# Optimization experiments

Hardware: AMD Instinct MI355X
Metric: run time of the kernel (lower is better)

The kernel has to match this reference:

```python
import jax, jax.numpy as jnp
import numpy as np
import math

E = 1024
H = 16
D = E // H  # head_dim = 64


def setup_inputs() -> dict:
    key = jax.random.key(0)
    ks = jax.random.split(key, 12)
    B, N = 2, 2048
    x = jax.random.normal(ks[0], (B, N, E), dtype=jnp.float32)
    region_mask = jax.random.randint(ks[1], (B, N), 0, 2).astype(jnp.float32)
    attn_mask = jax.random.randint(ks[2], (B, N, N), 0, 2).astype(bool)
    std = 0.02
    Wq = jax.random.normal(ks[3], (E, E), dtype=jnp.float32) * std
    Wk = jax.random.normal(ks[4], (E, E), dtype=jnp.float32) * std
    Wv = jax.random.normal(ks[5], (E, E), dtype=jnp.float32) * std
    Wo = jax.random.normal(ks[6], (E, E), dtype=jnp.float32) * std
    bq = jnp.zeros((E,), jnp.float32)
    bk = jnp.zeros((E,), jnp.float32)
    bv = jnp.zeros((E,), jnp.float32)
    bo = jnp.zeros((E,), jnp.float32)
    region_bias = jax.random.normal(ks[7], (1, H, 1, 1), dtype=jnp.float32) * std
    return {"x": x, "region_mask": region_mask, "attn_mask": attn_mask,
            "Wq": Wq, "bq": bq, "Wk": Wk, "bk": bk, "Wv": Wv, "bv": bv,
            "Wo": Wo, "bo": bo, "region_bias": region_bias}


def reference(x, region_mask, attn_mask, Wq, bq, Wk, bk, Wv, bv, Wo, bo, region_bias):
    B, N, _ = x.shape
    # projections (torch Linear: y = x @ W.T + b), split heads -> (B, H, N, D)
    def split_heads(y):
        return y.reshape(B, N, H, D).transpose(0, 2, 1, 3)
    q = split_heads(x @ Wq.T + bq)
    k = split_heads(x @ Wk.T + bk)
    v = split_heads(x @ Wv.T + bv)
    # eager scores (B, H, N, N)
    scores = jnp.einsum('bhqd,bhkd->bhqk', q, k) / math.sqrt(D)
    # additive regional bias: (1,H,1,1) * (B,1,N,1) broadcasts over keys
    scores = scores + region_bias * region_mask[:, None, :, None]
    # masked_fill(attn_mask, -inf); mask is (B,N,N) -> (B,1,N,N)
    scores = jnp.where(attn_mask[:, None, :, :], -jnp.inf, scores)
    w = jax.nn.softmax(scores, axis=-1)  # dropout is identity in eval
    out = jnp.einsum('bhqk,bhkd->bhqd', w, v)
    out = out.transpose(0, 2, 1, 3).reshape(B, N, E)
    return out @ Wo.T + bo
```

## Files before the change

### kernel.cpp

```cpp
#include <hip/hip_runtime.h>
#include <hip/hip_bf16.h>
#include <stdint.h>

typedef __hip_bfloat16 bf16;
typedef unsigned long long u64;
typedef __attribute__((ext_vector_type(4))) float f32x4;
typedef __attribute__((ext_vector_type(8))) short short8;

#define MFMA16 __builtin_amdgcn_mfma_f32_16x16x32_bf16

constexpr int Bc = 2, Nc = 2048, Ec = 1024, Hc = 16, Dc = 64;
constexpr int Mc = Bc * Nc;
constexpr int Kc = Ec;

constexpr size_t OFF_XB   = 256;
constexpr size_t SZ_XE    = (size_t)Mc * Ec * 2;
constexpr size_t SZ_W     = (size_t)Ec * Ec * 2;
constexpr size_t OFF_WQB  = OFF_XB  + SZ_XE;
constexpr size_t OFF_WKB  = OFF_WQB + SZ_W;
constexpr size_t OFF_WVB  = OFF_WKB + SZ_W;
constexpr size_t OFF_WOB  = OFF_WVB + SZ_W;
constexpr size_t OFF_QB   = OFF_WOB + SZ_W;
constexpr size_t OFF_KB   = OFF_QB  + SZ_XE;
constexpr size_t OFF_VTB  = OFF_KB  + SZ_XE;
constexpr size_t OFF_OB   = OFF_VTB + SZ_XE;
constexpr size_t OFF_MP   = OFF_OB  + SZ_XE;

#define QSCALE 0.18033688f

__device__ __forceinline__ void gld16(const void* g, void* l) {
  __builtin_amdgcn_global_load_lds((const __attribute__((address_space(1))) void*)g,
                                   (__attribute__((address_space(3))) void*)l,
                                   16, 0, 0);
}

__device__ __forceinline__ float fexp2(float x) {
#if __has_builtin(__builtin_amdgcn_exp2f)
  return __builtin_amdgcn_exp2f(x);
#else
  float r; asm("v_exp_f32 %0, %1" : "=v"(r) : "v"(x)); return r;
#endif
}

__device__ __forceinline__ unsigned cvt2(float a, float b) {
  __hip_bfloat162 h = __float22bfloat162_rn(float2{a, b});
  return *reinterpret_cast<unsigned*>(&h);
}

__device__ __forceinline__ unsigned nib4(unsigned x) {
  const unsigned b = ((x & 0x7F7F7F7Fu) + 0x7F7F7F7Fu) | x;
  return ((b >> 7) & 1u) | ((b >> 14) & 2u) | ((b >> 21) & 4u) | ((b >> 28) & 8u);
}

__global__ __launch_bounds__(256)
void prep(const unsigned char* __restrict__ mbytes,
          const float* __restrict__ x,  const float* __restrict__ wq,
          const float* __restrict__ wk, const float* __restrict__ wv,
          const float* __restrict__ wo,
          u64* __restrict__ packed,
          uint2* __restrict__ xb,  uint2* __restrict__ wqb,
          uint2* __restrict__ wkb, uint2* __restrict__ wvb,
          uint2* __restrict__ wob)
{
  if (blockIdx.x < 512) {
    __shared__ int found;
    if (threadIdx.x == 0) found = 0;
    __syncthreads();
    int loc = 0;
    for (int i = threadIdx.x; i < 4096; i += 256)
      if ((i & 3) && mbytes[i] == 1) loc = 1;
    if (loc) atomicOr(&found, 1);
    __syncthreads();
    const bool bytem = (found != 0);

    const int widx = blockIdx.x * 256 + threadIdx.x;
    u64 bits = 0;
    if (bytem) {
      const uint4* src = (const uint4*)(mbytes + (size_t)widx * 64);
#pragma unroll
      for (int i = 0; i < 4; ++i) {
        const uint4 v = src[i];
        bits |= (u64)nib4(v.x) << (16 * i + 0);
        bits |= (u64)nib4(v.y) << (16 * i + 4);
        bits |= (u64)nib4(v.z) << (16 * i + 8);
        bits |= (u64)nib4(v.w) << (16 * i + 12);
      }
    } else {
      const uint4* src = (const uint4*)mbytes + (size_t)widx * 16;
#pragma unroll
      for (int i = 0; i < 16; ++i) {
        const uint4 v = src[i];
        const unsigned n = (v.x != 0 ? 1u : 0u) | (v.y != 0 ? 2u : 0u) |
                           (v.z != 0 ? 4u : 0u) | (v.w != 0 ? 8u : 0u);
        bits |= (u64)n << (4 * i);
      }
    }
    packed[widx] = bits;
    return;
  }
  const long XG = (long)Mc * Ec / 4;
  const long WG = (long)Ec * Ec / 4;
  const long total = XG + 4 * WG;
  const long nthr = (long)(gridDim.x - 512) * 256;
  for (long g = (long)(blockIdx.x - 512) * 256 + threadIdx.x; g < total; g += nthr) {
    const float* src; uint2* dst; long r;
    if (g < XG)              { src = x;  dst = xb;  r = g; }
    else if (g < XG + WG)    { src = wq; dst = wqb; r = g - XG; }
    else if (g < XG + 2*WG)  { src = wk; dst = wkb; r = g - XG - WG; }
    else if (g < XG + 3*WG)  { src = wv; dst = wvb; r = g - XG - 2*WG; }
    else                     { src = wo; dst = wob; r = g - XG - 3*WG; }
    float4 v = reinterpret_cast<const float4*>(src)[r];
    uint2 o;
    o.x = cvt2(v.x, v.y);
    o.y = cvt2(v.z, v.w);
    dst[r] = o;
  }
}

__global__ __launch_bounds__(256)
void gemm_qkv(const bf16* __restrict__ xb,
              const bf16* __restrict__ wq, const bf16* __restrict__ wk,
              const bf16* __restrict__ wv,
              const float* __restrict__ bq, const float* __restrict__ bk,
              const float* __restrict__ bv,
              bf16* __restrict__ Q, bf16* __restrict__ Ko, bf16* __restrict__ VT)
{
  __shared__ bf16 As[2][128 * 64];
  __shared__ bf16 Bs[2][3][64 * 64];
  const int bm = blockIdx.x >> 4, bn = blockIdx.x & 15;
  const int t = threadIdx.x, lane = t & 63, w = t >> 6;
  const int wr = w >> 1, wc = w & 1;
  const int llo = lane & 15, lhi = lane >> 4;
  const int srow = t >> 3, schunk = t & 7;
  const int sswz = schunk ^ (srow & 7);
  const bf16* aSrc  = xb + (size_t)(bm * 128 + srow) * Kc + sswz * 8;
  const bf16* bSrc0 = wq + (size_t)(bn * 64 + srow) * Kc + sswz * 8;
  const bf16* bSrc1 = wk + (size_t)(bn * 64 + srow) * Kc + sswz * 8;
  const bf16* bSrc2 = wv + (size_t)(bn * 64 + srow) * Kc + sswz * 8;

  f32x4 acc[3][4][2] = {};

  auto stage = [&](int buf, int kt) {
    char* ldsA = (char*)As[buf] + w * 1024;
#pragma unroll
    for (int i = 0; i < 4; ++i)
      gld16(aSrc + (size_t)i * 32 * Kc + kt, ldsA + i * 4096);
#pragma unroll
    for (int s = 0; s < 3; ++s) {
      const bf16* bs = s == 0 ? bSrc0 : (s == 1 ? bSrc1 : bSrc2);
      char* ldsB = (char*)Bs[buf][s] + w * 1024;
      gld16(bs + kt, ldsB);
      gld16(bs + (size_t)32 * Kc + kt, ldsB + 4096);
    }
  };

  stage(0, 0);
  __syncthreads();

  for (int kti = 0; kti < Kc / 64; ++kti) {
    const int cur = kti & 1;
    if (kti + 1 < Kc / 64) stage(cur ^ 1, (kti + 1) * 64);
    const char* Asc = (const char*)As[cur];
#pragma unroll
    for (int kk = 0; kk < 2; ++kk) {
      const int chunk = (kk * 4 + lhi) ^ (lane & 7);
      short8 af[4];
#pragma unroll
      for (int i = 0; i < 4; ++i) {
        const int rowa = wr * 64 + i * 16 + llo;
        af[i] = *(const short8*)(Asc + rowa * 128 + chunk * 16);
      }
#pragma unroll
      for (int s = 0; s < 3; ++s) {
        const char* Bsc = (const char*)Bs[cur][s];
        const int rowb0 = wc * 32 + llo;
        short8 bg0 = *(const short8*)(Bsc + rowb0 * 128 + chunk * 16);
        short8 bg1 = *(const short8*)(Bsc + (rowb0 + 16) * 128 + chunk * 16);
#pragma unroll
        for (int i = 0; i < 4; ++i) {
          acc[s][i][0] = MFMA16(af[i], bg0, acc[s][i][0], 0, 0, 0);
          acc[s][i][1] = MFMA16(af[i], bg1, acc[s][i][1], 0, 0, 0);
        }
      }
    }
    __syncthreads();
  }

#pragma unroll
  for (int s = 0; s < 3; ++s) {
    const float* bias = s == 0 ? bq : (s == 1 ? bk : bv);
#pragma unroll
    for (int i = 0; i < 4; ++i)
#pragma unroll
      for (int j = 0; j < 2; ++j)
#pragma unroll
        for (int r = 0; r < 4; ++r) {
          const int m = bm * 128 + wr * 64 + i * 16 + lhi * 4 + r;
          const int e = bn * 64 + wc * 32 + j * 16 + llo;
          float v = acc[s][i][j][r] + bias[e];
          if (s == 0) {
            Q[(size_t)m * Ec + e] = __float2bfloat16(v * QSCALE);
          } else if (s == 1) {
            Ko[(size_t)m * Ec + e] = __float2bfloat16(v);
          } else {
            const int b = m >> 11, n = m & 2047, h = e >> 6, d = e & 63;
            VT[(((size_t)(b * Hc + h)) * Dc + d) * Nc + n] = __float2bfloat16(v);
          }
        }
  }
}

template<int BN>
__device__ __forceinline__ void gemm_core(const bf16* __restrict__ A,
                                          const bf16* __restrict__ Bw,
                                          int bm, int bn,
                                          bf16* As0, bf16* As1,
                                          bf16* Bs0, bf16* Bs1,
                                          f32x4 (&acc)[4][BN / 32])
{
  constexpr int NJ = BN / 32;
  const int t = threadIdx.x, lane = t & 63, w = t >> 6;
  const int wr = w >> 1, wc = w & 1;
  const int llo = lane & 15, lhi = lane >> 4;
  const int srow = t >> 3, schunk = t & 7;
  const int sswz = schunk ^ (srow & 7);
  const bf16* aSrc = A  + (size_t)(bm * 128 + srow) * Kc + sswz * 8;
  const bf16* bSrc = Bw + (size_t)(bn * BN  + srow) * Kc + sswz * 8;

  auto stage = [&](bf16* Asb, bf16* Bsb, int kt) {
    char* ldsA = (char*)Asb + w * 1024;
    char* ldsB = (char*)Bsb + w * 1024;
#pragma unroll
    for (int i = 0; i < 4; ++i)
      gld16(aSrc + (size_t)i * 32 * Kc + kt, ldsA + i * 4096);
#pragma unroll
    for (int i = 0; i < BN / 32; ++i)
      gld16(bSrc + (size_t)i * 32 * Kc + kt, ldsB + i * 4096);
  };

  stage(As0, Bs0, 0);
  __syncthreads();

  for (int kti = 0; kti < Kc / 64; ++kti) {
    const bool even = !(kti & 1);
    const char* Asc = (const char*)(even ? As0 : As1);
    const char* Bsc = (const char*)(even ? Bs0 : Bs1);
    if (kti + 1 < Kc / 64)
      stage(even ? As1 : As0, even ? Bs1 : Bs0, (kti + 1) * 64);
#pragma unroll
    for (int kk = 0; kk < 2; ++kk) {
      short8 af[4], bg[NJ];
      const int chunk = (kk * 4 + lhi) ^ (lane & 7);
#pragma unroll
      for (int i = 0; i < 4; ++i) {
        const int rowa = wr * 64 + i * 16 + llo;
        af[i] = *(const short8*)(Asc + rowa * 128 + chunk * 16);
      }
#pragma unroll
      for (int j = 0; j < NJ; ++j) {
        const int rowb = wc * (BN / 2) + j * 16 + llo;
        bg[j] = *(const short8*)(Bsc + rowb * 128 + chunk * 16);
      }
#pragma unroll
      for (int i = 0; i < 4; ++i)
#pragma unroll
        for (int j = 0; j < NJ; ++j)
          acc[i][j] = MFMA16(af[i], bg[j], acc[i][j], 0, 0, 0);
    }
    __syncthreads();
  }
}

__global__ __launch_bounds__(256)
void gemm_out(const bf16* __restrict__ ob, const bf16* __restrict__ wo,
              const float* __restrict__ bo, float* __restrict__ out)
{
  __shared__ bf16 As[2][128 * 64], Bs[2][64 * 64];
  const int bm = blockIdx.x >> 4, bn = blockIdx.x & 15;
  f32x4 acc[4][2] = {};
  gemm_core<64>(ob, wo, bm, bn, As[0], As[1], Bs[0], Bs[1], acc);

  const int t = threadIdx.x, lane = t & 63, w = t >> 6;
  const int wr = w >> 1, wc = w & 1;
  const int llo = lane & 15, lhi = lane >> 4;
#pragma unroll
  for (int i = 0; i < 4; ++i)
#pragma unroll
    for (int j = 0; j < 2; ++j)
#pragma unroll
      for (int r = 0; r < 4; ++r) {
        const int m = bm * 128 + wr * 64 + i * 16 + lhi * 4 + r;
        const int e = bn * 64 + wc * 32 + j * 16 + llo;
        out[(size_t)m * Ec + e] = acc[i][j][r] + bo[e];
      }
}

__global__ __launch_bounds__(512, 4)
void flash_attn(const bf16* __restrict__ Q, const bf16* __restrict__ Kb,
                const bf16* __restrict__ VT, const u64* __restrict__ mpack,
                bf16* __restrict__ O)
{
  __shared__ bf16 Ks[2][64 * 64];
  __shared__ bf16 Vs[2][64 * 64];
  __shared__ bf16 Ps[8][16 * 64];
  const int t = threadIdx.x, lane = t & 63, w = t >> 6;
  const int bh = blockIdx.x >> 4, qt = blockIdx.x & 15;
  const int b = bh >> 4, h = bh & 15;
  const int q0 = qt * 128 + w * 16;
  const int llo = lane & 15, lhi = lane >> 4;
  const int swz = (lane & 7) << 4;

  short8 aq0, aq1;
  {
    const bf16* qb = Q + ((size_t)(b * Nc + q0 + llo)) * Ec + h * Dc + lhi * 8;
    aq0 = *(const short8*)qb;
    aq1 = *(const short8*)(qb + 32);
  }

  const short8 kOnes = {16256,16256,16256,16256,16256,16256,16256,16256};
  const f32x4 fz = {};
  f32x4 oacc[4] = {};
  f32x4 lacc = {};

  const int srow = t >> 3, schunk = t & 7;
  const int sswz = schunk ^ (srow & 7);
  const bf16* kSrc = Kb + ((size_t)(b * Nc + srow)) * Ec + h * Dc + sswz * 8;
  const bf16* vSrc = VT + ((size_t)(bh * Dc + srow)) * Nc + sswz * 8;

  const u64* mrow = mpack + ((size_t)(b * Nc) + q0 + llo) * (Nc / 64);

  auto stage = [&](int buf, int kt) {
    gld16(kSrc + (size_t)kt * Ec, (char*)Ks[buf] + w * 1024);
    gld16(vSrc + kt,              (char*)Vs[buf] + w * 1024);
  };

  char* prow = (char*)Ps[w] + llo * 128;

  auto body = [&](const char* KsC, const char* VsC, u64 mw) {
    f32x4 s[4];
    __builtin_amdgcn_s_setprio(1);
#pragma unroll
    for (int f = 0; f < 4; ++f) {
      const int row = f * 16 + llo;
      short8 kb0 = *(const short8*)(KsC + row * 128 + (((0 + lhi) * 16) ^ swz));
      short8 kb1 = *(const short8*)(KsC + row * 128 + (((4 + lhi) * 16) ^ swz));
      s[f] = MFMA16(kb0, aq0, fz, 0, 0, 0);
      s[f] = MFMA16(kb1, aq1, s[f], 0, 0, 0);
    }
    __builtin_amdgcn_s_setprio(0);

    const unsigned mlo = (unsigned)(mw >> (lhi * 4));
    const unsigned mhi = (unsigned)(mw >> (lhi * 4 + 32));
#pragma unroll
    for (int f = 0; f < 4; ++f) {
      const unsigned mf = (f < 2 ? (mlo >> (f * 16)) : (mhi >> ((f - 2) * 16)));
#pragma unroll
      for (int r = 0; r < 4; ++r) {
        const float p = fexp2(s[f][r]);
        s[f][r] = ((mf >> r) & 1u) ? 0.f : p;
      }
    }

#pragma unroll
    for (int f = 0; f < 4; ++f) {
      uint2 pk;
      pk.x = cvt2(s[f][0], s[f][1]);
      pk.y = cvt2(s[f][2], s[f][3]);
      *(uint2*)(prow + ((f * 32 + lhi * 8) ^ swz)) = pk;
    }
    asm volatile("s_waitcnt lgkmcnt(0)" ::: "memory");

    short8 pa0 = *(const short8*)(prow + ((0 * 64 + lhi * 16) ^ swz));
    short8 pa1 = *(const short8*)(prow + ((1 * 64 + lhi * 16) ^ swz));

    __builtin_amdgcn_s_setprio(1);
#pragma unroll
    for (int df = 0; df < 4; ++df) {
      const int row = df * 16 + llo;
      short8 vb0 = *(const short8*)(VsC + row * 128 + (((0 + lhi) * 16) ^ swz));
      short8 vb1 = *(const short8*)(VsC + row * 128 + (((4 + lhi) * 16) ^ swz));
      oacc[df] = MFMA16(pa0, vb0, oacc[df], 0, 0, 0);
      oacc[df] = MFMA16(pa1, vb1, oacc[df], 0, 0, 0);
    }
    lacc = MFMA16(pa0, kOnes, lacc, 0, 0, 0);
    lacc = MFMA16(pa1, kOnes, lacc, 0, 0, 0);
    __builtin_amdgcn_s_setprio(0);
  };

  stage(0, 0);
  __syncthreads();
  u64 mw = mrow[0];

  for (int ti = 0; ti < Nc / 64; ti += 2) {
    if (ti + 1 < Nc / 64) stage(1, (ti + 1) * 64);
    const u64 mwB = (ti + 1 < Nc / 64) ? mrow[ti + 1] : 0;
    body((const char*)Ks[0], (const char*)Vs[0], mw);
    __syncthreads();
    if (ti + 2 < Nc / 64) stage(0, (ti + 2) * 64);
    const u64 mwA = (ti + 2 < Nc / 64) ? mrow[ti + 2] : 0;
    body((const char*)Ks[1], (const char*)Vs[1], mwB);
    __syncthreads();
    mw = mwA;
  }

  float inv[4];
#pragma unroll
  for (int r = 0; r < 4; ++r) inv[r] = 1.0f / lacc[r];
#pragma unroll
  for (int df = 0; df < 4; ++df)
#pragma unroll
    for (int r = 0; r < 4; ++r) {
      const int q = q0 + lhi * 4 + r;
      const int e = h * Dc + df * 16 + llo;
      O[((size_t)(b * Nc + q)) * Ec + e] = __float2bfloat16(oacc[df][r] * inv[r]);
    }
}

extern "C" void kernel_launch(void* const* d_in, const int* in_sizes, int n_in,
                              void* d_out, int out_size, void* d_ws, size_t ws_size,
                              hipStream_t stream)
{
  (void)in_sizes; (void)n_in; (void)out_size; (void)ws_size;
  const float* x  = (const float*)d_in[0];
  const void* mask = d_in[2];
  const float* Wq = (const float*)d_in[3];
  const float* bq = (const float*)d_in[4];
  const float* Wk = (const float*)d_in[5];
  const float* bk = (const float*)d_in[6];
  const float* Wv = (const float*)d_in[7];
  const float* bv = (const float*)d_in[8];
  const float* Wo = (const float*)d_in[9];
  const float* bo = (const float*)d_in[10];
  float* out = (float*)d_out;
  char* ws = (char*)d_ws;

  bf16* XB  = (bf16*)(ws + OFF_XB);
  bf16* WQB = (bf16*)(ws + OFF_WQB);
  bf16* WKB = (bf16*)(ws + OFF_WKB);
  bf16* WVB = (bf16*)(ws + OFF_WVB);
  bf16* WOB = (bf16*)(ws + OFF_WOB);
  bf16* QB  = (bf16*)(ws + OFF_QB);
  bf16* KB  = (bf16*)(ws + OFF_KB);
  bf16* VTB = (bf16*)(ws + OFF_VTB);
  bf16* OB  = (bf16*)(ws + OFF_OB);
  u64*  MP  = (u64*)(ws + OFF_MP);

  prep<<<512 + 1280, 256, 0, stream>>>((const unsigned char*)mask,
                                       x, Wq, Wk, Wv, Wo, MP,
                                       (uint2*)XB, (uint2*)WQB, (uint2*)WKB,
                                       (uint2*)WVB, (uint2*)WOB);
  gemm_qkv<<<512, 256, 0, stream>>>(XB, WQB, WKB, WVB, bq, bk, bv, QB, KB, VTB);
  flash_attn<<<512, 512, 0, stream>>>(QB, KB, VTB, MP, OB);
  gemm_out<<<512, 256, 0, stream>>>(OB, WOB, bo, out);
}
```

Before: 133.9 us.

## Software-pipeline flash attention: overlap PV of tile i with QK of tile i+1

New measurement: 128.1 us (median of 2 runs). 4.3% less time.

```diff
diff --git a/kernel.cpp b/kernel.cpp
--- a/kernel.cpp
+++ b/kernel.cpp
@@ -302,7 +302,8 @@
 {
   __shared__ bf16 Ks[2][64 * 64];
   __shared__ bf16 Vs[2][64 * 64];
-  __shared__ bf16 Ps[8][16 * 64];
+  __shared__ bf16 Ps[8][2][16 * 64];
+  constexpr int NT = Nc / 64;
   const int t = threadIdx.x, lane = t & 63, w = t >> 6;
   const int bh = blockIdx.x >> 4, qt = blockIdx.x & 15;
   const int b = bh >> 4, h = bh & 15;
@@ -329,14 +330,17 @@
 
   const u64* mrow = mpack + ((size_t)(b * Nc) + q0 + llo) * (Nc / 64);
 
-  auto stage = [&](int buf, int kt) {
+  auto stageK = [&](int buf, int kt) {
     gld16(kSrc + (size_t)kt * Ec, (char*)Ks[buf] + w * 1024);
-    gld16(vSrc + kt,              (char*)Vs[buf] + w * 1024);
-  };
-
-  char* prow = (char*)Ps[w] + llo * 128;
-
-  auto body = [&](const char* KsC, const char* VsC, u64 mw) {
+  };
+  auto stageV = [&](int buf, int kt) {
+    gld16(vSrc + kt, (char*)Vs[buf] + w * 1024);
+  };
+
+  char* pw0 = (char*)Ps[w][0] + llo * 128;
+  char* pw1 = (char*)Ps[w][1] + llo * 128;
+
+  auto qk_part = [&](const char* KsC, char* pwW, u64 mw) {
     f32x4 s[4];
     __builtin_amdgcn_s_setprio(1);
 #pragma unroll
@@ -366,13 +370,13 @@
       uint2 pk;
       pk.x = cvt2(s[f][0], s[f][1]);
       pk.y = cvt2(s[f][2], s[f][3]);
-      *(uint2*)(prow + ((f * 32 + lhi * 8) ^ swz)) = pk;
-    }
-    asm volatile("s_waitcnt lgkmcnt(0)" ::: "memory");
-
-    short8 pa0 = *(const short8*)(prow + ((0 * 64 + lhi * 16) ^ swz));
-    short8 pa1 = *(const short8*)(prow + ((1 * 64 + lhi * 16) ^ swz));
-
+      *(uint2*)(pwW + ((f * 32 + lhi * 8) ^ swz)) = pk;
+    }
+  };
+
+  auto pv_part = [&](const char* pwR, const char* VsC) {
+    short8 pa0 = *(const short8*)(pwR + ((0 * 64 + lhi * 16) ^ swz));
+    short8 pa1 = *(const short8*)(pwR + ((1 * 64 + lhi * 16) ^ swz));
     __builtin_amdgcn_s_setprio(1);
 #pragma unroll
     for (int df = 0; df < 4; ++df) {
@@ -387,21 +391,33 @@
     __builtin_amdgcn_s_setprio(0);
   };
 
-  stage(0, 0);
+  stageK(0, 0);
   __syncthreads();
-  u64 mw = mrow[0];
-
-  for (int ti = 0; ti < Nc / 64; ti += 2) {
-    if (ti + 1 < Nc / 64) stage(1, (ti + 1) * 64);
-    const u64 mwB = (ti + 1 < Nc / 64) ? mrow[ti + 1] : 0;
-    body((const char*)Ks[0], (const char*)Vs[0], mw);
-    __syncthreads();
-    if (ti + 2 < Nc / 64) stage(0, (ti + 2) * 64);
-    const u64 mwA = (ti + 2 < Nc / 64) ? mrow[ti + 2] : 0;
-    body((const char*)Ks[1], (const char*)Vs[1], mwB);
-    __syncthreads();
-    mw = mwA;
-  }
+
+  stageK(1, 64);
+  stageV(0, 0);
+  qk_part((const char*)Ks[0], pw0, mrow[0]);
+  __syncthreads();
+
+  for (int ti = 1; ti + 1 < NT; ti += 2) {
+    stageK(0, (ti + 1) * 64);
+    stageV(1, ti * 64);
+    pv_part(pw0, (const char*)Vs[0]);
+    qk_part((const char*)Ks[1], pw1, mrow[ti]);
+    __syncthreads();
+    if (ti + 2 < NT) stageK(1, (ti + 2) * 64);
+    stageV(0, (ti + 1) * 64);
+    pv_part(pw1, (const char*)Vs[1]);
+    qk_part((const char*)Ks[0], pw0, mrow[ti + 1]);
+    __syncthreads();
+  }
+
+  stageV(1, (NT - 1) * 64);
+  pv_part(pw0, (const char*)Vs[0]);
+  qk_part((const char*)Ks[1], pw1, mrow[NT - 1]);
+  __syncthreads();
+
+  pv_part(pw1, (const char*)Vs[1]);
 
   float inv[4];
 #pragma unroll
```
